# Kernel optimization log

Measured on AMD Instinct MI355X. Metric: run time of the kernel, lower is better.

## Reference

```python
import jax, jax.numpy as jnp
import numpy as np
import math

EMBED_DIM = 256
NUM_HEADS = 8
FFN_DIM = 1024
EPS = 1e-5


def layer_norm(x, g, b):
    mu = jnp.mean(x, axis=-1, keepdims=True)
    var = jnp.var(x, axis=-1, keepdims=True)
    return (x - mu) / jnp.sqrt(var + EPS) * g + b


def setup_inputs() -> dict:
    key = jax.random.key(0)
    ks = jax.random.split(key, 10)
    B, L, D, F = 4, 2048, EMBED_DIM, FFN_DIM
    x = jax.random.normal(ks[0], (B, L, D), dtype=jnp.float32)
    mask = jnp.ones((B, L), dtype=jnp.int32)
    # FFN params (PyTorch Linear default-ish scale)
    W1 = jax.random.normal(ks[1], (D, F), dtype=jnp.float32) / np.sqrt(D)
    b1 = jnp.zeros((F,), dtype=jnp.float32)
    W2 = jax.random.normal(ks[2], (F, D), dtype=jnp.float32) / np.sqrt(F)
    b2 = jnp.zeros((D,), dtype=jnp.float32)
    g1 = jnp.ones((D,), dtype=jnp.float32)
    be1 = jnp.zeros((D,), dtype=jnp.float32)
    g2 = jnp.ones((D,), dtype=jnp.float32)
    be2 = jnp.zeros((D,), dtype=jnp.float32)
    return {"x": x, "mask": mask, "W1": W1, "b1": b1, "W2": W2, "b2": b2,
            "g1": g1, "be1": be1, "g2": g2, "be2": be2}


def quantum_attention(x, mask):
    B, L, D = x.shape
    H, dk = NUM_HEADS, D // NUM_HEADS
    xh = x.reshape(B, L, H, dk).transpose(0, 2, 1, 3)  # [B,H,L,dk]
    # per-token mean over batch and heads -> [L, dk]
    m = jnp.mean(xh, axis=(0, 1))
    # closed form of the single-qubit RX circuit: P(|1>) = sin^2(angle/2)
    dot = m @ m.T  # [L, L]
    ang = jnp.clip(dot, -math.pi, math.pi)
    scores = jnp.sin(ang * 0.5) ** 2  # [L, L], shared across B and H
    attn = jnp.broadcast_to(scores[None, None], (B, H, L, L))
    attn = jnp.where(mask[:, None, None, :] == 0, -1e9, attn)
    attn = jax.nn.softmax(attn, axis=-1)
    out = jnp.einsum('bhij,bhjd->bhid', attn, xh)  # values are xh itself
    return out.transpose(0, 2, 1, 3).reshape(B, L, D)


def reference(x, mask, W1, b1, W2, b2, g1, be1, g2, be2):
    attn_out = quantum_attention(x, mask)
    h = layer_norm(x + attn_out, g1, be1)
    ffn = jax.nn.relu(h @ W1 + b1) @ W2 + b2
    return layer_norm(h + ffn, g2, be2)
```

## Files before the change

### kernel.cpp

```cpp
#include <hip/hip_runtime.h>
#include <hip/hip_bf16.h>


#define B_ 4
#define L_ 2048
#define D_ 256
#define F_ 1024
#define PI_F 3.14159265358979323846f

typedef __bf16 bf16x8 __attribute__((ext_vector_type(8)));
typedef float floatx4 __attribute__((ext_vector_type(4)));
typedef unsigned short ushortx4 __attribute__((ext_vector_type(4)));

__device__ __forceinline__ unsigned short f2bf(float f) {
    unsigned int u = __float_as_uint(f);
    u = (u + 0x7FFFu + ((u >> 16) & 1u)) >> 16;
    return (unsigned short)u;
}
__device__ __forceinline__ float bf2f(unsigned short u) {
    union { unsigned int i; float f; } v; v.i = ((unsigned int)u) << 16; return v.f;
}

__device__ __forceinline__ void async_cp16(unsigned short* lds, const unsigned short* g) {
    __builtin_amdgcn_global_load_lds(
        (const __attribute__((address_space(1))) unsigned int*)g,
        (__attribute__((address_space(3))) unsigned int*)lds, 16, 0, 0);
}

__global__ __launch_bounds__(256) void k_prep(const float* __restrict__ x,
                                              const float* __restrict__ W1,
                                              const float* __restrict__ W2,
                                              const int* __restrict__ mask,
                                              unsigned short* __restrict__ mb,
                                              unsigned short* __restrict__ XmT,
                                              unsigned short* __restrict__ W1T,
                                              unsigned short* __restrict__ W2T) {
    __shared__ float tile[32][33];
    int r = blockIdx.x, t = threadIdx.x;
    if (r >= 2560) {
        if (r < 2816) {
            int idx = (r - 2560) * 256 + t;
            int l = idx >> 5, k = idx & 31;
            float s = 0.f;
#pragma unroll
            for (int b = 0; b < B_; b++) {
                const float* xp = x + ((size_t)(b * L_ + l)) * D_ + k;
#pragma unroll
                for (int h = 0; h < 8; h++) s += xp[h * 32];
            }
            mb[idx] = f2bf(s * (1.f / 32.f));
        } else {
#pragma unroll
            for (int c = 0; c < 32; c++) {
                int e = c * 256 + t;
                int b = e >> 11, j = e & (L_ - 1);
                XmT[(size_t)(1024 + b) * L_ + j] = mask[b * L_ + j] ? 0x3F80 : 0;
            }
        }
        return;
    }
    const float* in; unsigned short* outp; int R, C; const int* mrow = nullptr; size_t bo = 0;
    int bx, by;
    if (r < 2048) {
        int z = r >> 9, rem = r & 511; by = rem >> 3; bx = rem & 7;
        in = x; outp = XmT; R = L_; C = 256; bo = (size_t)z * R * C; mrow = mask + z * L_;
    } else if (r < 2304) {
        int rem = r - 2048; bx = rem & 31; by = rem >> 5;
        in = W1; outp = W1T; R = 256; C = 1024;
    } else {
        int rem = r - 2304; bx = rem & 7; by = rem >> 3;
        in = W2; outp = W2T; R = 1024; C = 256;
    }
    int r0 = by * 32, c0 = bx * 32;
    int tx = t & 31, ty = t >> 5;
#pragma unroll
    for (int rr = 0; rr < 4; rr++) {
        int rw = ty + rr * 8;
        tile[rw][tx] = in[bo + (size_t)(r0 + rw) * C + c0 + tx];
    }
    float mfac = 1.f;
    if (mrow) mfac = mrow[r0 + tx] ? 1.f : 0.f;
    __syncthreads();
#pragma unroll
    for (int rr = 0; rr < 4; rr++) {
        int c = ty + rr * 8;
        outp[bo + (size_t)(c0 + c) * R + r0 + tx] = f2bf(tile[tx][c] * mfac);
    }
}

__global__ __launch_bounds__(256) void k_scores_mfma(const unsigned short* __restrict__ mb,
                                                     unsigned short* __restrict__ E) {
    const int t = threadIdx.x, lane = t & 63, wid = t >> 6;
    const int wm = (wid >> 1) * 64, wn = (wid & 1) * 32;
    const int lr = lane & 15, lq = lane >> 4;
    int m0 = blockIdx.y * 128, n0 = blockIdx.x * 64;
    bf16x8 af[4], bfr[2];
#pragma unroll
    for (int i = 0; i < 4; i++)
        af[i] = *(const bf16x8*)(mb + (size_t)(m0 + wm + i * 16 + lr) * 32 + lq * 8);
#pragma unroll
    for (int j = 0; j < 2; j++)
        bfr[j] = *(const bf16x8*)(mb + (size_t)(n0 + wn + j * 16 + lr) * 32 + lq * 8);
    floatx4 acc[4][2];
#pragma unroll
    for (int i = 0; i < 4; i++)
#pragma unroll
        for (int j = 0; j < 2; j++) {
            acc[i][j] = (floatx4){0.f, 0.f, 0.f, 0.f};
            acc[i][j] = __builtin_amdgcn_mfma_f32_16x16x32_bf16(af[i], bfr[j], acc[i][j], 0, 0, 0);
        }
#pragma unroll
    for (int i = 0; i < 4; i++)
#pragma unroll
        for (int j = 0; j < 2; j++)
#pragma unroll
            for (int r = 0; r < 4; r++) {
                int row = m0 + wm + i * 16 + lq * 4 + r;
                int col = n0 + wn + j * 16 + lr;
                float d = fminf(fmaxf(acc[i][j][r], -PI_F), PI_F);
                float sn = __sinf(0.5f * d);
                E[(size_t)row * L_ + col] = f2bf(__expf(sn * sn));
            }
}

__global__ __launch_bounds__(256) void k_av(const unsigned short* __restrict__ E,
                                            const unsigned short* __restrict__ XmT,
                                            unsigned short* __restrict__ Cb) {
    __shared__ __align__(16) unsigned short sA[2][128 * 64];
    __shared__ __align__(16) unsigned short sB[2][64 * 64];
    const int t = threadIdx.x, lane = t & 63, wid = t >> 6;
    const int wm = (wid >> 1) * 64, wn = (wid & 1) * 32;
    const int lr = lane & 15, lq = lane >> 4;
    const int lrow = lane >> 3, lseg = lane & 7;

    int bid = blockIdx.x;
    int swz = (bid & 7) * 34 + (bid >> 3);
    int m0 = (swz / 17) * 128, n0 = (swz % 17) * 64;

    const unsigned short* Ag[4]; int sAoff[4];
#pragma unroll
    for (int q = 0; q < 4; q++) {
        int rl = wid * 32 + q * 8 + lrow;
        Ag[q] = E + (size_t)(m0 + rl) * L_ + ((lseg - rl) & 7) * 8;
        sAoff[q] = (wid * 32 + q * 8) * 64;
    }
    const unsigned short* Bg[2]; int sBoff[2];
#pragma unroll
    for (int q = 0; q < 2; q++) {
        int rl = wid * 16 + q * 8 + lrow;
        Bg[q] = XmT + (size_t)(n0 + rl) * L_ + ((lseg - rl) & 7) * 8;
        sBoff[q] = (wid * 16 + q * 8) * 64;
    }
    int arot[4], aroff[4], brot[2], broff[2];
#pragma unroll
    for (int i = 0; i < 4; i++) { int ar = wm + i * 16 + lr; aroff[i] = ar * 64; arot[i] = lq + ar; }
#pragma unroll
    for (int j = 0; j < 2; j++) { int br = wn + j * 16 + lr; broff[j] = br * 64; brot[j] = lq + br; }

    floatx4 acc[4][2];
#pragma unroll
    for (int i = 0; i < 4; i++)
#pragma unroll
        for (int j = 0; j < 2; j++) acc[i][j] = (floatx4){0.f, 0.f, 0.f, 0.f};

    auto stage = [&](unsigned short* dA, unsigned short* dB, int k0) {
#pragma unroll
        for (int q = 0; q < 4; q++) async_cp16(dA + sAoff[q], Ag[q] + k0);
#pragma unroll
        for (int q = 0; q < 2; q++) async_cp16(dB + sBoff[q], Bg[q] + k0);
    };
    auto compute = [&](const unsigned short* cA, const unsigned short* cB) {
#pragma unroll
        for (int s = 0; s < 2; s++) {
            bf16x8 af[4], bfr[2];
#pragma unroll
            for (int i = 0; i < 4; i++)
                af[i] = *(const bf16x8*)(cA + aroff[i] + ((s * 4 + arot[i]) & 7) * 8);
#pragma unroll
            for (int j = 0; j < 2; j++)
                bfr[j] = *(const bf16x8*)(cB + broff[j] + ((s * 4 + brot[j]) & 7) * 8);
#pragma unroll
            for (int i = 0; i < 4; i++)
#pragma unroll
                for (int j = 0; j < 2; j++)
                    acc[i][j] = __builtin_amdgcn_mfma_f32_16x16x32_bf16(af[i], bfr[j], acc[i][j], 0, 0, 0);
        }
    };

    stage(sA[0], sB[0], 0);
    __syncthreads();
    for (int st = 0; st < 32; st += 2) {
        stage(sA[1], sB[1], (st + 1) << 6);
        compute(sA[0], sB[0]);
        __syncthreads();
        if (st + 2 < 32) stage(sA[0], sB[0], (st + 2) << 6);
        compute(sA[1], sB[1]);
        __syncthreads();
    }
#pragma unroll
    for (int i = 0; i < 4; i++)
#pragma unroll
        for (int j = 0; j < 2; j++)
#pragma unroll
            for (int r = 0; r < 4; r++) {
                int row = m0 + wm + i * 16 + lq * 4 + r;
                int col = n0 + wn + j * 16 + lr;
                Cb[(size_t)row * 1088 + col] = f2bf(acc[i][j][r]);
            }
}

__global__ __launch_bounds__(256) void k_ln1(const float* __restrict__ x, const unsigned short* __restrict__ Cb,
                                             const float* __restrict__ g_, const float* __restrict__ be_,
                                             unsigned short* __restrict__ hb) {
    int t = threadIdx.x, wid = t >> 6, lane = t & 63;
    int tok = (blockIdx.x << 2) + wid;
    int b = tok >> 11, i = tok & (L_ - 1);
    float rs = bf2f(Cb[(size_t)i * 1088 + 1024 + b]);
    float4 xv = *(const float4*)(x + (size_t)tok * D_ + lane * 4);
    ushortx4 cv = *(const ushortx4*)(Cb + (size_t)i * 1088 + b * 256 + lane * 4);
    float v0 = xv.x + bf2f(cv.x) / rs;
    float v1 = xv.y + bf2f(cv.y) / rs;
    float v2 = xv.z + bf2f(cv.z) / rs;
    float v3 = xv.w + bf2f(cv.w) / rs;
    float s  = v0 + v1 + v2 + v3;
    float s2 = v0 * v0 + v1 * v1 + v2 * v2 + v3 * v3;
#pragma unroll
    for (int o = 1; o < 64; o <<= 1) { s += __shfl_xor(s, o); s2 += __shfl_xor(s2, o); }
    float mu = s * (1.f / 256.f);
    float var = s2 * (1.f / 256.f) - mu * mu;
    float r = rsqrtf(var + 1e-5f);
    float4 gv = *(const float4*)(g_ + lane * 4);
    float4 bv = *(const float4*)(be_ + lane * 4);
    ushortx4 o4;
    o4.x = f2bf((v0 - mu) * r * gv.x + bv.x);
    o4.y = f2bf((v1 - mu) * r * gv.y + bv.y);
    o4.z = f2bf((v2 - mu) * r * gv.z + bv.z);
    o4.w = f2bf((v3 - mu) * r * gv.w + bv.w);
    *(ushortx4*)(hb + (size_t)tok * D_ + lane * 4) = o4;
}

__global__ __launch_bounds__(256) void k_gemm1(const unsigned short* __restrict__ hb,
                                               const unsigned short* __restrict__ W1T,
                                               const float* __restrict__ b1, unsigned short* __restrict__ t1) {
    __shared__ __align__(16) unsigned short sA[2][128 * 64];
    __shared__ __align__(16) unsigned short sB[2][128 * 64];
    const int t = threadIdx.x, lane = t & 63, wid = t >> 6;
    const int wm = (wid >> 1) * 64, wn = (wid & 1) * 64;
    const int lr = lane & 15, lq = lane >> 4;
    const int lrow8 = lane >> 3, lseg = lane & 7;

    int bid = blockIdx.x;
    int swz = (bid & 7) * 64 + (bid >> 3);
    int m0 = (swz >> 3) * 128, n0 = (swz & 7) * 128;

    const unsigned short* Ag[4]; const unsigned short* Bg[4]; int soff[4];
#pragma unroll
    for (int q = 0; q < 4; q++) {
        int rl = q * 32 + wid * 8 + lrow8;
        int seg = (lseg - rl) & 7;
        Ag[q] = hb + (size_t)(m0 + rl) * 256 + seg * 8;
        Bg[q] = W1T + (size_t)(n0 + rl) * 256 + seg * 8;
        soff[q] = (q * 32 + wid * 8) * 64;
    }
    int arot[4], aroff[4], brot[4], broff[4];
#pragma unroll
    for (int i = 0; i < 4; i++) { int ar = wm + i * 16 + lr; aroff[i] = ar * 64; arot[i] = lq + ar; }
#pragma unroll
    for (int j = 0; j < 4; j++) { int br = wn + j * 16 + lr; broff[j] = br * 64; brot[j] = lq + br; }

    floatx4 acc[4][4];
#pragma unroll
    for (int i = 0; i < 4; i++)
#pragma unroll
        for (int j = 0; j < 4; j++) acc[i][j] = (floatx4){0.f, 0.f, 0.f, 0.f};

    auto stage = [&](unsigned short* dA, unsigned short* dB, int k0) {
#pragma unroll
        for (int q = 0; q < 4; q++) { async_cp16(dA + soff[q], Ag[q] + k0); async_cp16(dB + soff[q], Bg[q] + k0); }
    };
    auto compute = [&](const unsigned short* cA, const unsigned short* cB) {
#pragma unroll
        for (int s = 0; s < 2; s++) {
            bf16x8 af[4], bfr[4];
#pragma unroll
            for (int i = 0; i < 4; i++) af[i] = *(const bf16x8*)(cA + aroff[i] + ((s * 4 + arot[i]) & 7) * 8);
#pragma unroll
            for (int j = 0; j < 4; j++) bfr[j] = *(const bf16x8*)(cB + broff[j] + ((s * 4 + brot[j]) & 7) * 8);
#pragma unroll
            for (int i = 0; i < 4; i++)
#pragma unroll
                for (int j = 0; j < 4; j++)
                    acc[i][j] = __builtin_amdgcn_mfma_f32_16x16x32_bf16(af[i], bfr[j], acc[i][j], 0, 0, 0);
        }
    };

    stage(sA[0], sB[0], 0);
    __syncthreads();
    for (int st = 0; st < 4; st += 2) {
        stage(sA[1], sB[1], (st + 1) << 6);
        compute(sA[0], sB[0]);
        __syncthreads();
        if (st + 2 < 4) stage(sA[0], sB[0], (st + 2) << 6);
        compute(sA[1], sB[1]);
        __syncthreads();
    }
    float bb[4];
#pragma unroll
    for (int j = 0; j < 4; j++) bb[j] = b1[n0 + wn + j * 16 + lr];
#pragma unroll
    for (int i = 0; i < 4; i++)
#pragma unroll
        for (int j = 0; j < 4; j++) {
            int col = n0 + wn + j * 16 + lr;
#pragma unroll
            for (int r = 0; r < 4; r++) {
                int row = m0 + wm + i * 16 + lq * 4 + r;
                t1[(size_t)row * 1024 + col] = f2bf(fmaxf(acc[i][j][r] + bb[j], 0.f));
            }
        }
}

__global__ __launch_bounds__(256) void k_gemm2ln(const unsigned short* __restrict__ t1,
                                                 const unsigned short* __restrict__ W2T,
                                                 const float* __restrict__ b2,
                                                 const unsigned short* __restrict__ hb,
                                                 const float* __restrict__ g_, const float* __restrict__ be_,
                                                 float* __restrict__ out) {
    __shared__ __align__(16) unsigned short sA[2][32 * 64];
    __shared__ __align__(16) unsigned short sB[2][256 * 64];
    __shared__ float red[2][32][2];
    const int t = threadIdx.x, lane = t & 63, wid = t >> 6;
    const int wm = (wid >> 1) * 16, wn = (wid & 1) * 128;
    const int lr = lane & 15, lq = lane >> 4;
    const int lrow8 = lane >> 3, lseg = lane & 7;
    int m0 = blockIdx.x * 32;

    int arl = wid * 8 + lrow8;
    const unsigned short* Ag = t1 + (size_t)(m0 + arl) * 1024 + (((lseg - arl) & 7) * 8);
    int sAoff = (wid * 8) * 64;
    const unsigned short* Bg[8]; int sBoff[8];
#pragma unroll
    for (int q = 0; q < 8; q++) {
        int rl = q * 32 + wid * 8 + lrow8;
        Bg[q] = W2T + (size_t)rl * 1024 + (((lseg - rl) & 7) * 8);
        sBoff[q] = (q * 32 + wid * 8) * 64;
    }
    int aroff = (wm + lr) * 64, arot = lq + wm + lr;
    int brot[8], broff[8];
#pragma unroll
    for (int j = 0; j < 8; j++) { int br = wn + j * 16 + lr; broff[j] = br * 64; brot[j] = lq + br; }

    floatx4 acc[8];
#pragma unroll
    for (int j = 0; j < 8; j++) acc[j] = (floatx4){0.f, 0.f, 0.f, 0.f};

    auto stage = [&](unsigned short* dA, unsigned short* dB, int k0) {
        async_cp16(dA + sAoff, Ag + k0);
#pragma unroll
        for (int q = 0; q < 8; q++) async_cp16(dB + sBoff[q], Bg[q] + k0);
    };
    auto compute = [&](const unsigned short* cA, const unsigned short* cB) {
#pragma unroll
        for (int s = 0; s < 2; s++) {
            bf16x8 af = *(const bf16x8*)(cA + aroff + ((s * 4 + arot) & 7) * 8);
#pragma unroll
            for (int j = 0; j < 8; j++) {
                bf16x8 bfr = *(const bf16x8*)(cB + broff[j] + ((s * 4 + brot[j]) & 7) * 8);
                acc[j] = __builtin_amdgcn_mfma_f32_16x16x32_bf16(af, bfr, acc[j], 0, 0, 0);
            }
        }
    };

    stage(sA[0], sB[0], 0);
    __syncthreads();
    for (int st = 0; st < 16; st += 2) {
        stage(sA[1], sB[1], (st + 1) << 6);
        compute(sA[0], sB[0]);
        __syncthreads();
        if (st + 2 < 16) stage(sA[0], sB[0], (st + 2) << 6);
        compute(sA[1], sB[1]);
        __syncthreads();
    }
    float psum[4], psq[4];
#pragma unroll
    for (int r = 0; r < 4; r++) { psum[r] = 0.f; psq[r] = 0.f; }
#pragma unroll
    for (int j = 0; j < 8; j++) {
        int col = wn + j * 16 + lr;
        float bv = b2[col];
#pragma unroll
        for (int r = 0; r < 4; r++) {
            int row = m0 + wm + lq * 4 + r;
            float v = acc[j][r] + bv + bf2f(hb[(size_t)row * 256 + col]);
            acc[j][r] = v;
            psum[r] += v; psq[r] += v * v;
        }
    }
#pragma unroll
    for (int o = 1; o < 16; o <<= 1) {
#pragma unroll
        for (int r = 0; r < 4; r++) { psum[r] += __shfl_xor(psum[r], o); psq[r] += __shfl_xor(psq[r], o); }
    }
    if (lr == 0) {
#pragma unroll
        for (int r = 0; r < 4; r++) {
            int lrow = wm + lq * 4 + r;
            red[wid & 1][lrow][0] = psum[r];
            red[wid & 1][lrow][1] = psq[r];
        }
    }
    __syncthreads();
#pragma unroll
    for (int r = 0; r < 4; r++) {
        int lrow = wm + lq * 4 + r;
        float s = red[0][lrow][0] + red[1][lrow][0];
        float s2 = red[0][lrow][1] + red[1][lrow][1];
        float mu = s * (1.f / 256.f);
        float var = s2 * (1.f / 256.f) - mu * mu;
        float rc = rsqrtf(var + 1e-5f);
        int row = m0 + lrow;
#pragma unroll
        for (int j = 0; j < 8; j++) {
            int col = wn + j * 16 + lr;
            out[(size_t)row * 256 + col] = (acc[j][r] - mu) * rc * g_[col] + be_[col];
        }
    }
}

extern "C" void kernel_launch(void* const* d_in, const int* in_sizes, int n_in,
                              void* d_out, int out_size, void* d_ws, size_t ws_size,
                              hipStream_t stream) {
    const float* x   = (const float*)d_in[0];
    const int*  mask = (const int*)d_in[1];
    const float* W1  = (const float*)d_in[2];
    const float* b1  = (const float*)d_in[3];
    const float* W2  = (const float*)d_in[4];
    const float* b2  = (const float*)d_in[5];
    const float* g1  = (const float*)d_in[6];
    const float* be1 = (const float*)d_in[7];
    const float* g2  = (const float*)d_in[8];
    const float* be2 = (const float*)d_in[9];
    float* out = (float*)d_out;

    char* w = (char*)d_ws;
    unsigned short* mb_   = (unsigned short*)w;  w += 65536 * 2;
    unsigned short* E_    = (unsigned short*)w;  w += (size_t)L_ * L_ * 2;
    unsigned short* XmT_  = (unsigned short*)w;  w += (size_t)1088 * L_ * 2;
    unsigned short* W1T_  = (unsigned short*)w;  w += 262144 * 2;
    unsigned short* W2T_  = (unsigned short*)w;  w += 262144 * 2;
    unsigned short* Cb_   = (unsigned short*)w;  w += (size_t)L_ * 1088 * 2;
    unsigned short* hb_   = (unsigned short*)w;  w += (size_t)8192 * 256 * 2;
    unsigned short* t1_   = (unsigned short*)w;  w += (size_t)8192 * 1024 * 2;

    k_prep<<<2817, 256, 0, stream>>>(x, W1, W2, mask, mb_, XmT_, W1T_, W2T_);
    k_scores_mfma<<<dim3(32, 16), 256, 0, stream>>>(mb_, E_);
    k_av<<<272, 256, 0, stream>>>(E_, XmT_, Cb_);
    k_ln1<<<2048, 256, 0, stream>>>(x, Cb_, g1, be1, hb_);
    k_gemm1<<<512, 256, 0, stream>>>(hb_, W1T_, b1, t1_);
    k_gemm2ln<<<256, 256, 0, stream>>>(t1_, W2T_, b2, hb_, g2, be2, out);
}
```

Baseline: 149.2 us.

## Triple-buffer LDS pipelines with explicit vmcnt waits in GEMM kernels

Reworks the async global-to-LDS staging in k_av and k_gemm2ln into a three-deep ring buffer, and restructures k_gemm1 into an unrolled two-buffer sequence. The pipelines use explicit s_waitcnt vmcnt counts and raw s_barrier with sched barriers instead of __syncthreads. This keeps two tiles of loads in flight while computing, aiming to hide global memory latency better. The cost is larger LDS footprint, which may lower occupancy (k_gemm2ln now uses about 108KB). It also relies on exact vmcnt accounting for correctness.

```diff
diff --git a/kernel.cpp b/kernel.cpp
--- a/kernel.cpp
+++ b/kernel.cpp
@@ -11,6 +11,10 @@
 typedef __bf16 bf16x8 __attribute__((ext_vector_type(8)));
 typedef float floatx4 __attribute__((ext_vector_type(4)));
 typedef unsigned short ushortx4 __attribute__((ext_vector_type(4)));
+
+#define WAIT_VM(n) asm volatile("s_waitcnt vmcnt(" #n ")" ::: "memory")
+#define SCHED0() __builtin_amdgcn_sched_barrier(0)
+#define BARRIER() do { SCHED0(); __builtin_amdgcn_s_barrier(); SCHED0(); } while (0)
 
 __device__ __forceinline__ unsigned short f2bf(float f) {
     unsigned int u = __float_as_uint(f);
@@ -126,8 +130,7 @@
 __global__ __launch_bounds__(256) void k_av(const unsigned short* __restrict__ E,
                                             const unsigned short* __restrict__ XmT,
                                             unsigned short* __restrict__ Cb) {
-    __shared__ __align__(16) unsigned short sA[2][128 * 64];
-    __shared__ __align__(16) unsigned short sB[2][64 * 64];
+    __shared__ __align__(16) unsigned short sbuf[3][128 * 64 + 64 * 64];
     const int t = threadIdx.x, lane = t & 63, wid = t >> 6;
     const int wm = (wid >> 1) * 64, wn = (wid & 1) * 32;
     const int lr = lane & 15, lq = lane >> 4;
@@ -149,13 +152,13 @@
     for (int q = 0; q < 2; q++) {
         int rl = wid * 16 + q * 8 + lrow;
         Bg[q] = XmT + (size_t)(n0 + rl) * L_ + ((lseg - rl) & 7) * 8;
-        sBoff[q] = (wid * 16 + q * 8) * 64;
+        sBoff[q] = 8192 + (wid * 16 + q * 8) * 64;
     }
     int arot[4], aroff[4], brot[2], broff[2];
 #pragma unroll
     for (int i = 0; i < 4; i++) { int ar = wm + i * 16 + lr; aroff[i] = ar * 64; arot[i] = lq + ar; }
 #pragma unroll
-    for (int j = 0; j < 2; j++) { int br = wn + j * 16 + lr; broff[j] = br * 64; brot[j] = lq + br; }
+    for (int j = 0; j < 2; j++) { int br = wn + j * 16 + lr; broff[j] = 8192 + br * 64; brot[j] = lq + br; }
 
     floatx4 acc[4][2];
 #pragma unroll
@@ -163,22 +166,22 @@
 #pragma unroll
         for (int j = 0; j < 2; j++) acc[i][j] = (floatx4){0.f, 0.f, 0.f, 0.f};
 
-    auto stage = [&](unsigned short* dA, unsigned short* dB, int k0) {
-#pragma unroll
-        for (int q = 0; q < 4; q++) async_cp16(dA + sAoff[q], Ag[q] + k0);
-#pragma unroll
-        for (int q = 0; q < 2; q++) async_cp16(dB + sBoff[q], Bg[q] + k0);
-    };
-    auto compute = [&](const unsigned short* cA, const unsigned short* cB) {
+    auto stage = [&](unsigned short* base, int k0) {
+#pragma unroll
+        for (int q = 0; q < 4; q++) async_cp16(base + sAoff[q], Ag[q] + k0);
+#pragma unroll
+        for (int q = 0; q < 2; q++) async_cp16(base + sBoff[q], Bg[q] + k0);
+    };
+    auto compute = [&](const unsigned short* base) {
 #pragma unroll
         for (int s = 0; s < 2; s++) {
             bf16x8 af[4], bfr[2];
 #pragma unroll
             for (int i = 0; i < 4; i++)
-                af[i] = *(const bf16x8*)(cA + aroff[i] + ((s * 4 + arot[i]) & 7) * 8);
+                af[i] = *(const bf16x8*)(base + aroff[i] + ((s * 4 + arot[i]) & 7) * 8);
 #pragma unroll
             for (int j = 0; j < 2; j++)
-                bfr[j] = *(const bf16x8*)(cB + broff[j] + ((s * 4 + brot[j]) & 7) * 8);
+                bfr[j] = *(const bf16x8*)(base + broff[j] + ((s * 4 + brot[j]) & 7) * 8);
 #pragma unroll
             for (int i = 0; i < 4; i++)
 #pragma unroll
@@ -187,16 +190,24 @@
         }
     };
 
-    stage(sA[0], sB[0], 0);
-    __syncthreads();
-    for (int st = 0; st < 32; st += 2) {
-        stage(sA[1], sB[1], (st + 1) << 6);
-        compute(sA[0], sB[0]);
-        __syncthreads();
-        if (st + 2 < 32) stage(sA[0], sB[0], (st + 2) << 6);
-        compute(sA[1], sB[1]);
-        __syncthreads();
-    }
+    unsigned short *p0 = sbuf[0], *p1 = sbuf[1], *p2 = sbuf[2];
+    stage(p0, 0); stage(p1, 64); stage(p2, 128);
+    WAIT_VM(12); BARRIER();
+    for (int p = 0; p < 29; ++p) {
+        compute(p0);
+        BARRIER();
+        stage(p0, (p + 3) << 6);
+        WAIT_VM(12); BARRIER();
+        unsigned short* tmp = p0; p0 = p1; p1 = p2; p2 = tmp;
+    }
+    compute(p0);
+    BARRIER();
+    WAIT_VM(6); BARRIER();
+    compute(p1);
+    BARRIER();
+    WAIT_VM(0); BARRIER();
+    compute(p2);
+
 #pragma unroll
     for (int i = 0; i < 4; i++)
 #pragma unroll
@@ -242,8 +253,7 @@
 __global__ __launch_bounds__(256) void k_gemm1(const unsigned short* __restrict__ hb,
                                                const unsigned short* __restrict__ W1T,
                                                const float* __restrict__ b1, unsigned short* __restrict__ t1) {
-    __shared__ __align__(16) unsigned short sA[2][128 * 64];
-    __shared__ __align__(16) unsigned short sB[2][128 * 64];
+    __shared__ __align__(16) unsigned short sbuf[2][128 * 64 + 128 * 64];
     const int t = threadIdx.x, lane = t & 63, wid = t >> 6;
     const int wm = (wid >> 1) * 64, wn = (wid & 1) * 64;
     const int lr = lane & 15, lq = lane >> 4;
@@ -253,20 +263,21 @@
     int swz = (bid & 7) * 64 + (bid >> 3);
     int m0 = (swz >> 3) * 128, n0 = (swz & 7) * 128;
 
-    const unsigned short* Ag[4]; const unsigned short* Bg[4]; int soff[4];
+    const unsigned short* Ag[4]; const unsigned short* Bg[4]; int aoff[4], boff4[4];
 #pragma unroll
     for (int q = 0; q < 4; q++) {
         int rl = q * 32 + wid * 8 + lrow8;
         int seg = (lseg - rl) & 7;
         Ag[q] = hb + (size_t)(m0 + rl) * 256 + seg * 8;
         Bg[q] = W1T + (size_t)(n0 + rl) * 256 + seg * 8;
-        soff[q] = (q * 32 + wid * 8) * 64;
+        aoff[q] = (q * 32 + wid * 8) * 64;
+        boff4[q] = 8192 + (q * 32 + wid * 8) * 64;
     }
     int arot[4], aroff[4], brot[4], broff[4];
 #pragma unroll
     for (int i = 0; i < 4; i++) { int ar = wm + i * 16 + lr; aroff[i] = ar * 64; arot[i] = lq + ar; }
 #pragma unroll
-    for (int j = 0; j < 4; j++) { int br = wn + j * 16 + lr; broff[j] = br * 64; brot[j] = lq + br; }
+    for (int j = 0; j < 4; j++) { int br = wn + j * 16 + lr; broff[j] = 8192 + br * 64; brot[j] = lq + br; }
 
     floatx4 acc[4][4];
 #pragma unroll
@@ -274,18 +285,18 @@
 #pragma unroll
         for (int j = 0; j < 4; j++) acc[i][j] = (floatx4){0.f, 0.f, 0.f, 0.f};
 
-    auto stage = [&](unsigned short* dA, unsigned short* dB, int k0) {
-#pragma unroll
-        for (int q = 0; q < 4; q++) { async_cp16(dA + soff[q], Ag[q] + k0); async_cp16(dB + soff[q], Bg[q] + k0); }
-    };
-    auto compute = [&](const unsigned short* cA, const unsigned short* cB) {
+    auto stage = [&](unsigned short* base, int k0) {
+#pragma unroll
+        for (int q = 0; q < 4; q++) { async_cp16(base + aoff[q], Ag[q] + k0); async_cp16(base + boff4[q], Bg[q] + k0); }
+    };
+    auto compute = [&](const unsigned short* base) {
 #pragma unroll
         for (int s = 0; s < 2; s++) {
             bf16x8 af[4], bfr[4];
 #pragma unroll
-            for (int i = 0; i < 4; i++) af[i] = *(const bf16x8*)(cA + aroff[i] + ((s * 4 + arot[i]) & 7) * 8);
-#pragma unroll
-            for (int j = 0; j < 4; j++) bfr[j] = *(const bf16x8*)(cB + broff[j] + ((s * 4 + brot[j]) & 7) * 8);
+            for (int i = 0; i < 4; i++) af[i] = *(const bf16x8*)(base + aroff[i] + ((s * 4 + arot[i]) & 7) * 8);
+#pragma unroll
+            for (int j = 0; j < 4; j++) bfr[j] = *(const bf16x8*)(base + broff[j] + ((s * 4 + brot[j]) & 7) * 8);
 #pragma unroll
             for (int i = 0; i < 4; i++)
 #pragma unroll
@@ -294,16 +305,22 @@
         }
     };
 
-    stage(sA[0], sB[0], 0);
-    __syncthreads();
-    for (int st = 0; st < 4; st += 2) {
-        stage(sA[1], sB[1], (st + 1) << 6);
-        compute(sA[0], sB[0]);
-        __syncthreads();
-        if (st + 2 < 4) stage(sA[0], sB[0], (st + 2) << 6);
-        compute(sA[1], sB[1]);
-        __syncthreads();
-    }
+    unsigned short *pa = sbuf[0], *pb = sbuf[1];
+    stage(pa, 0); stage(pb, 64);
+    WAIT_VM(8); BARRIER();
+    compute(pa);
+    BARRIER();
+    stage(pa, 128);
+    WAIT_VM(8); BARRIER();
+    compute(pb);
+    BARRIER();
+    stage(pb, 192);
+    WAIT_VM(8); BARRIER();
+    compute(pa);
+    BARRIER();
+    WAIT_VM(0); BARRIER();
+    compute(pb);
+
     float bb[4];
 #pragma unroll
     for (int j = 0; j < 4; j++) bb[j] = b1[n0 + wn + j * 16 + lr];
@@ -326,8 +343,7 @@
                                                  const unsigned short* __restrict__ hb,
                                                  const float* __restrict__ g_, const float* __restrict__ be_,
                                                  float* __restrict__ out) {
-    __shared__ __align__(16) unsigned short sA[2][32 * 64];
-    __shared__ __align__(16) unsigned short sB[2][256 * 64];
+    __shared__ __align__(16) unsigned short sbuf[3][32 * 64 + 256 * 64];
     __shared__ float red[2][32][2];
     const int t = threadIdx.x, lane = t & 63, wid = t >> 6;
     const int wm = (wid >> 1) * 16, wn = (wid & 1) * 128;
@@ -343,44 +359,52 @@
     for (int q = 0; q < 8; q++) {
         int rl = q * 32 + wid * 8 + lrow8;
         Bg[q] = W2T + (size_t)rl * 1024 + (((lseg - rl) & 7) * 8);
-        sBoff[q] = (q * 32 + wid * 8) * 64;
+        sBoff[q] = 2048 + (q * 32 + wid * 8) * 64;
     }
     int aroff = (wm + lr) * 64, arot = lq + wm + lr;
     int brot[8], broff[8];
 #pragma unroll
-    for (int j = 0; j < 8; j++) { int br = wn + j * 16 + lr; broff[j] = br * 64; brot[j] = lq + br; }
+    for (int j = 0; j < 8; j++) { int br = wn + j * 16 + lr; broff[j] = 2048 + br * 64; brot[j] = lq + br; }
 
     floatx4 acc[8];
 #pragma unroll
     for (int j = 0; j < 8; j++) acc[j] = (floatx4){0.f, 0.f, 0.f, 0.f};
 
-    auto stage = [&](unsigned short* dA, unsigned short* dB, int k0) {
-        async_cp16(dA + sAoff, Ag + k0);
-#pragma unroll
-        for (int q = 0; q < 8; q++) async_cp16(dB + sBoff[q], Bg[q] + k0);
-    };
-    auto compute = [&](const unsigned short* cA, const unsigned short* cB) {
+    auto stage = [&](unsigned short* base, int k0) {
+        async_cp16(base + sAoff, Ag + k0);
+#pragma unroll
+        for (int q = 0; q < 8; q++) async_cp16(base + sBoff[q], Bg[q] + k0);
+    };
+    auto compute = [&](const unsigned short* base) {
 #pragma unroll
         for (int s = 0; s < 2; s++) {
-            bf16x8 af = *(const bf16x8*)(cA + aroff + ((s * 4 + arot) & 7) * 8);
+            bf16x8 af = *(const bf16x8*)(base + aroff + ((s * 4 + arot) & 7) * 8);
 #pragma unroll
             for (int j = 0; j < 8; j++) {
-                bf16x8 bfr = *(const bf16x8*)(cB + broff[j] + ((s * 4 + brot[j]) & 7) * 8);
+                bf16x8 bfr = *(const bf16x8*)(base + broff[j] + ((s * 4 + brot[j]) & 7) * 8);
                 acc[j] = __builtin_amdgcn_mfma_f32_16x16x32_bf16(af, bfr, acc[j], 0, 0, 0);
             }
         }
     };
 
-    stage(sA[0], sB[0], 0);
-    __syncthreads();
-    for (int st = 0; st < 16; st += 2) {
-        stage(sA[1], sB[1], (st + 1) << 6);
-        compute(sA[0], sB[0]);
-        __syncthreads();
-        if (st + 2 < 16) stage(sA[0], sB[0], (st + 2) << 6);
-        compute(sA[1], sB[1]);
-        __syncthreads();
-    }
+    unsigned short *p0 = sbuf[0], *p1 = sbuf[1], *p2 = sbuf[2];
+    stage(p0, 0); stage(p1, 64); stage(p2, 128);
+    WAIT_VM(18); BARRIER();
+    for (int p = 0; p < 13; ++p) {
+        compute(p0);
+        BARRIER();
+        stage(p0, (p + 3) << 6);
+        WAIT_VM(18); BARRIER();
+        unsigned short* tmp = p0; p0 = p1; p1 = p2; p2 = tmp;
+    }
+    compute(p0);
+    BARRIER();
+    WAIT_VM(9); BARRIER();
+    compute(p1);
+    BARRIER();
+    WAIT_VM(0); BARRIER();
+    compute(p2);
+
     float psum[4], psq[4];
 #pragma unroll
     for (int r = 0; r < 4; r++) { psum[r] = 0.f; psq[r] = 0.f; }
```

Result: faster. 139.9 us (-6.2%).
